# Kernel optimization log

Hardware: AMD Instinct MI355X
Metric: run time of the kernel (lower is better)

The kernel has to match this reference:

```python
import jax, jax.numpy as jnp
import numpy as np

D_MODEL, D_STATE, BATCH, SEQ = 512, 32, 8, 4096

def _hippo(n):
    i = np.arange(n)[:, None].astype(np.float64)
    j = np.arange(n)[None, :].astype(np.float64)
    P = np.where(i > j, np.sqrt(2 * i + 1) * np.sqrt(2 * j + 1), 0.0)
    P = P + np.diag(np.arange(1, n + 1).astype(np.float64))
    return (-P).astype(np.float32)

def setup_inputs() -> dict:
    key = jax.random.key(0)
    k0, k1, k2, k3 = jax.random.split(key, 4)
    x = jax.random.normal(k0, (BATCH, SEQ, D_MODEL), dtype=jnp.float32)
    A = jnp.asarray(_hippo(D_STATE))
    B = jax.random.normal(k1, (D_STATE, D_MODEL), dtype=jnp.float32) / np.float32(np.sqrt(D_MODEL))
    C = jax.random.normal(k2, (D_MODEL, D_STATE), dtype=jnp.float32) / np.float32(np.sqrt(D_STATE))
    D = jnp.ones((D_MODEL,), dtype=jnp.float32)
    log_dt = jnp.zeros((D_MODEL,), dtype=jnp.float32)
    W_out = jax.random.normal(k3, (D_MODEL, D_MODEL), dtype=jnp.float32) / np.float32(np.sqrt(D_MODEL))
    b_out = jnp.zeros((D_MODEL,), dtype=jnp.float32)
    return {"x": x, "A": A, "B": B, "C": C, "D": D, "log_dt": log_dt, "W_out": W_out, "b_out": b_out}

def reference(x, A, B, C, D, log_dt, W_out, b_out):
    # x: (b, s, d). S4 layer with bilinear discretization and tanh recurrence.
    n = A.shape[0]
    dt = jnp.mean(jnp.clip(jnp.exp(log_dt), 1e-4, 1.0))  # scalar dt.mean()
    I = jnp.eye(n, dtype=x.dtype)
    inv_term = jnp.linalg.inv(I - 0.5 * dt * A)
    A_bar = (I + 0.5 * dt * A) @ inv_term          # (n, n)
    B_bar = dt * (inv_term @ B)                    # (n, d)
    # Precompute input projection for all timesteps (vectorized):
    uB = jnp.einsum('bsd,nd->bsn', x, B_bar)       # (b, s, n)
    s0 = jnp.zeros((x.shape[0], n), dtype=x.dtype)
    def step(state, ub_t):
        state = jnp.tanh(state @ A_bar.T + ub_t)   # (b, n)
        return state, state
    final_state, states = jax.lax.scan(step, s0, jnp.swapaxes(uB, 0, 1))
    states = jnp.swapaxes(states, 0, 1)            # (b, s, n)
    y = jnp.einsum('bsn,dn->bsd', states, C) + x * D
    y = y @ W_out.T + b_out                        # output_proj (dropout = eval identity)
    return y, final_state
```

## Files before the change

### kernel.cpp

```cpp
#include <hip/hip_runtime.h>
#include <hip/hip_bf16.h>

#define D_MODEL 512
#define D_STATE 32
#define BATCH 8
#define SEQ 4096
#define MROWS (BATCH * SEQ)

typedef __bf16 bf16;
typedef __bf16 bf16x4 __attribute__((ext_vector_type(4)));
typedef __bf16 bf16x8 __attribute__((ext_vector_type(8)));
typedef float f32x4 __attribute__((ext_vector_type(4)));
typedef _Float16 half_t;
typedef _Float16 half2_t __attribute__((ext_vector_type(2)));
typedef _Float16 half8 __attribute__((ext_vector_type(8)));

#define CHUNK 16
#define BURN 80
#define NCHUNK (SEQ / CHUNK)

__device__ __forceinline__ bf16x8 cvt8(const f32x4 a, const f32x4 b) {
  bf16x8 h;
  h[0] = (bf16)a[0]; h[1] = (bf16)a[1]; h[2] = (bf16)a[2]; h[3] = (bf16)a[3];
  h[4] = (bf16)b[0]; h[5] = (bf16)b[1]; h[6] = (bf16)b[2]; h[7] = (bf16)b[3];
  return h;
}

__global__ __launch_bounds__(256) void k_pre(
    const float* __restrict__ A, const float* __restrict__ C, const float* __restrict__ Dv,
    const float* __restrict__ log_dt, const float* __restrict__ W,
    float* __restrict__ A_bar, float* __restrict__ XTs,
    bf16* __restrict__ CW, bf16* __restrict__ WD) {
  __shared__ float Xs[32][32];
  const int bid = blockIdx.x, t = threadIdx.x;
  float* Xf = &Xs[0][0];

  if (bid == 0) {
    {
      float v0 = __expf(log_dt[t]);
      float v1 = __expf(log_dt[t + 256]);
      v0 = fminf(fmaxf(v0, 1e-4f), 1.0f);
      v1 = fminf(fmaxf(v1, 1e-4f), 1.0f);
      Xf[t] = v0 + v1;
    }
    __syncthreads();
    for (int s2 = 128; s2 > 0; s2 >>= 1) {
      if (t < s2) Xf[t] += Xf[t + s2];
      __syncthreads();
    }
    const float dtv = Xf[0] * (1.0f / 512.0f);
    __syncthreads();
    {
      const int i0 = 4 * t;
      const f32x4 av = *(const f32x4*)(A + i0);
      f32x4 mv;
#pragma unroll
      for (int q = 0; q < 4; q++) {
        const int r = (i0 + q) >> 5, c = (i0 + q) & 31;
        mv[q] = (r == c ? 1.0f : 0.0f) - 0.5f * dtv * av[q];
      }
      *(f32x4*)(Xf + i0) = mv;
    }
    __syncthreads();
    if (t < 32) {
      const int j = t;
      float xcol[32];
#pragma unroll
      for (int i = 0; i < 32; i++) {
        float s0 = 0.f, s1 = 0.f, s2 = 0.f, s3 = 0.f;
#pragma unroll
        for (int k = 0; k < 32; k += 4) {
          if (k < i)     s0 -= Xf[i * 32 + k]     * xcol[k];
          if (k + 1 < i) s1 -= Xf[i * 32 + k + 1] * xcol[k + 1];
          if (k + 2 < i) s2 -= Xf[i * 32 + k + 2] * xcol[k + 2];
          if (k + 3 < i) s3 -= Xf[i * 32 + k + 3] * xcol[k + 3];
        }
        const float num = (i == j ? 1.0f : 0.0f) + ((s0 + s1) + (s2 + s3));
        xcol[i] = (i >= j) ? num / Xf[i * 32 + i] : 0.0f;
      }
#pragma unroll
      for (int i = 0; i < 32; i++) Xs[i][j] = xcol[i];
    }
    __syncthreads();
    {
      const int i0 = 4 * t;
      const int r = t >> 3;
      f32x4 ov;
#pragma unroll
      for (int q = 0; q < 4; q++) {
        const int c = (i0 + q) & 31;
        float s = 0.f;
#pragma unroll
        for (int k = 0; k < 32; k++) {
          const float p2 = (r == k ? 1.0f : 0.0f) + 0.5f * dtv * A[r * 32 + k];
          s = fmaf(p2, Xf[k * 32 + c], s);
        }
        ov[q] = s;
      }
      *(f32x4*)(A_bar + i0) = ov;
    }
#pragma unroll
    for (int i = 0; i < 4; i++) {
      const int idx = t + i * 256;
      const int k = idx >> 5, n = idx & 31;
      XTs[idx] = dtv * Xf[n * 32 + k];
    }
  } else if (bid <= 16) {
    const int w = t >> 6, lane = t & 63;
    const int l15 = lane & 15, kg = lane >> 4;
    const int m = w & 1, nf = w >> 1;
    const int eb = (bid - 1) * 32;
    const float* wp = W + (long)(eb + m * 16 + l15) * D_MODEL + kg * 8;
    const int ncol = nf * 16 + l15;
    f32x4 acc = (f32x4)(0.0f);
#pragma unroll 1
    for (int kt = 0; kt < 16; kt++) {
      const f32x4 w0 = *(const f32x4*)(wp + kt * 32);
      const f32x4 w1 = *(const f32x4*)(wp + kt * 32 + 4);
      const bf16x8 af = cvt8(w0, w1);
      bf16x8 bf;
#pragma unroll
      for (int j = 0; j < 8; j++)
        bf[j] = (bf16)C[(kt * 32 + kg * 8 + j) * D_STATE + ncol];
      acc = __builtin_amdgcn_mfma_f32_16x16x32_bf16(af, bf, acc, 0, 0, 0);
    }
#pragma unroll
    for (int jj = 0; jj < 4; jj++)
      CW[(eb + m * 16 + kg * 4 + jj) * D_STATE + ncol] = (bf16)acc[jj];
  } else {
#pragma unroll
    for (int jj = 0; jj < 16; jj++) {
      const int i = (bid - 17) * 16384 + jj * 1024 + t * 4;
      const f32x4 wv = *(const f32x4*)(W + i);
      const f32x4 dv = *(const f32x4*)(Dv + (i & 511));
      bf16x4 h;
#pragma unroll
      for (int q = 0; q < 4; q++) h[q] = (bf16)(wv[q] * dv[q]);
      *(bf16x4*)(WD + i) = h;
    }
  }
}

__device__ __forceinline__ void stage_x(const float* __restrict__ x, long rowbase,
                                        int kt, void* lds, int t) {
#pragma unroll
  for (int j = 0; j < 2; j++) {
    const int boff = j * 4096 + t * 16;
    const int r = boff >> 7;
    const int s = (boff >> 4) & 7;
    const int cb = (s ^ (r & 7)) << 4;
    const char* src = (const char*)(x + (rowbase + r) * D_MODEL) + kt * 128 + cb;
    const int udst = j * 4096 + ((t >> 6) << 10);
    __builtin_amdgcn_global_load_lds(
        (const __attribute__((address_space(1))) void*)src,
        (__attribute__((address_space(3))) void*)((char*)lds + udst), 16, 0, 0);
  }
}

__global__ __launch_bounds__(256, 2) void k_uB(
    const float* __restrict__ x, const float* __restrict__ B,
    const float* __restrict__ XTs,
    float* __restrict__ uB, bf16* __restrict__ xb) {
  __shared__ float xs[2][64 * 32];
  __shared__ float sXT[1024];
  __shared__ float srw[64 * 33];
  const int t = threadIdx.x, w = t >> 6, lane = t & 63;
  const int l15 = lane & 15, kg = lane >> 4;
  const long rowbase = (long)blockIdx.x * 64;

#pragma unroll
  for (int i = 0; i < 4; i++) sXT[t + i * 256] = XTs[t + i * 256];

  const int arow = w * 16 + l15;
  bf16* xo = xb + (rowbase + arow) * D_MODEL + kg * 8;
  const float* bp0 = B + l15 * D_MODEL + kg * 8;
  const float* bp1 = B + (16 + l15) * D_MODEL + kg * 8;
  const int ps0 = (((kg * 2) ^ (arow & 7)) << 2);
  const int ps1 = (((kg * 2 + 1) ^ (arow & 7)) << 2);
  const float* xsrow0 = &xs[0][arow * 32];
  const float* xsrow1 = &xs[1][arow * 32];

  f32x4 acc0 = (f32x4)(0.0f), acc1 = (f32x4)(0.0f);
  f32x4 cb0, cb1, cb2, cb3, nb0, nb1, nb2, nb3;

  stage_x(x, rowbase, 0, &xs[0][0], t);
  cb0 = *(const f32x4*)(bp0); cb1 = *(const f32x4*)(bp0 + 4);
  cb2 = *(const f32x4*)(bp1); cb3 = *(const f32x4*)(bp1 + 4);

#pragma unroll 1
  for (int kt = 0; kt < 16; kt++) {
    __syncthreads();
    if (kt < 15) {
      stage_x(x, rowbase, kt + 1, &xs[(kt + 1) & 1][0], t);
      const int o = (kt + 1) * 32;
      nb0 = *(const f32x4*)(bp0 + o); nb1 = *(const f32x4*)(bp0 + o + 4);
      nb2 = *(const f32x4*)(bp1 + o); nb3 = *(const f32x4*)(bp1 + o + 4);
    }
    const float* xr = (kt & 1) ? xsrow1 : xsrow0;
    const f32x4 a0 = *(const f32x4*)(xr + ps0);
    const f32x4 a1 = *(const f32x4*)(xr + ps1);
    const bf16x8 af = cvt8(a0, a1);
    *(bf16x8*)(xo + kt * 32) = af;
    const bf16x8 bh0 = cvt8(cb0, cb1);
    const bf16x8 bh1 = cvt8(cb2, cb3);
    bf16x8 bl0, bl1;
#pragma unroll
    for (int q = 0; q < 4; q++) {
      bl0[q]     = (bf16)(cb0[q] - (float)bh0[q]);
      bl0[q + 4] = (bf16)(cb1[q] - (float)bh0[q + 4]);
      bl1[q]     = (bf16)(cb2[q] - (float)bh1[q]);
      bl1[q + 4] = (bf16)(cb3[q] - (float)bh1[q + 4]);
    }
    acc0 = __builtin_amdgcn_mfma_f32_16x16x32_bf16(af, bh0, acc0, 0, 0, 0);
    acc0 = __builtin_amdgcn_mfma_f32_16x16x32_bf16(af, bl0, acc0, 0, 0, 0);
    acc1 = __builtin_amdgcn_mfma_f32_16x16x32_bf16(af, bh1, acc1, 0, 0, 0);
    acc1 = __builtin_amdgcn_mfma_f32_16x16x32_bf16(af, bl1, acc1, 0, 0, 0);
    cb0 = nb0; cb1 = nb1; cb2 = nb2; cb3 = nb3;
  }
#pragma unroll
  for (int jj = 0; jj < 4; jj++) {
    srw[(w * 16 + kg * 4 + jj) * 33 + l15]      = acc0[jj];
    srw[(w * 16 + kg * 4 + jj) * 33 + 16 + l15] = acc1[jj];
  }
  __syncthreads();
  {
    const int r = t & 63, ng = t >> 6;
    f32x4 u0 = (f32x4)(0.0f), u1 = (f32x4)(0.0f);
#pragma unroll
    for (int k = 0; k < 32; k++) {
      const float sv = srw[r * 33 + k];
      const f32x4 x0 = *(const f32x4*)&sXT[k * 32 + ng * 4];
      const f32x4 x1 = *(const f32x4*)&sXT[k * 32 + ng * 4 + 16];
#pragma unroll
      for (int q = 0; q < 4; q++) {
        u0[q] = fmaf(sv, x0[q], u0[q]);
        u1[q] = fmaf(sv, x1[q], u1[q]);
      }
    }
    float* up = uB + (rowbase + r) * D_STATE;
    *(f32x4*)(up + ng * 4) = u0;
    *(f32x4*)(up + ng * 4 + 16) = u1;
  }
}

__global__ void k_scan(const float* __restrict__ uB, const float* __restrict__ A_bar,
                       bf16* __restrict__ Sb, float* __restrict__ fs) {
  __shared__ half_t hs[256];
  const int t = threadIdx.x;
  const int g = t >> 5, n = t & 31;
  const int chain = blockIdx.x * 8 + g;
  const int b = chain >> 8;
  const int ch = chain & 255;
  const int cs = ch * CHUNK;
  const int t0 = cs - BURN;
  const int ce = cs + CHUNK;

  half2_t ah[16];
#pragma unroll
  for (int k = 0; k < 16; k++) {
    ah[k][0] = (half_t)A_bar[n * 32 + 2 * k];
    ah[k][1] = (half_t)A_bar[n * 32 + 2 * k + 1];
  }
#pragma unroll
  for (int k = 0; k < 16; k++) asm volatile("" : "+v"(ah[k]));

  const float* ub = uB + (long)b * SEQ * D_STATE + n;
  bf16* sp = Sb + ((long)b * SEQ + cs) * D_STATE + n;
  half_t* myslot = &hs[g * 32];

  float s = 0.f;
  float ubuf[8], unext[8];
#pragma unroll
  for (int i = 0; i < 8; i++) {
    const int tt = t0 + i;
    ubuf[i] = (tt >= 0) ? ub[(long)tt * D_STATE] : 0.f;
  }
  for (int tg = t0; tg < ce; tg += 8) {
    const int tn = tg + 8;
#pragma unroll
    for (int i = 0; i < 8; i++) {
      const int tt = tn + i;
      unext[i] = (tt >= 0 && tt < ce) ? ub[(long)tt * D_STATE] : 0.f;
    }
#pragma unroll
    for (int i = 0; i < 8; i++) {
      const int tt = tg + i;
      myslot[n] = (half_t)s;
      const half8 h0 = *(const half8*)(myslot + 0);
      const half8 h1 = *(const half8*)(myslot + 8);
      const half8 h2 = *(const half8*)(myslot + 16);
      const half8 h3 = *(const half8*)(myslot + 24);
      float acc0 = ubuf[i], acc1 = 0.f, acc2 = 0.f, acc3 = 0.f;
#if __has_builtin(__builtin_amdgcn_fdot2)
#pragma unroll
      for (int j = 0; j < 4; j++) {
        acc0 = __builtin_amdgcn_fdot2(ah[j],      ((const half2_t*)&h0)[j], acc0, false);
        acc1 = __builtin_amdgcn_fdot2(ah[4 + j],  ((const half2_t*)&h1)[j], acc1, false);
        acc2 = __builtin_amdgcn_fdot2(ah[8 + j],  ((const half2_t*)&h2)[j], acc2, false);
        acc3 = __builtin_amdgcn_fdot2(ah[12 + j], ((const half2_t*)&h3)[j], acc3, false);
      }
#else
#pragma unroll
      for (int j = 0; j < 4; j++) {
#pragma unroll
        for (int q = 0; q < 2; q++) {
          acc0 = fmaf((float)ah[j][q],      (float)((const half2_t*)&h0)[j][q], acc0);
          acc1 = fmaf((float)ah[4 + j][q],  (float)((const half2_t*)&h1)[j][q], acc1);
          acc2 = fmaf((float)ah[8 + j][q],  (float)((const half2_t*)&h2)[j][q], acc2);
          acc3 = fmaf((float)ah[12 + j][q], (float)((const half2_t*)&h3)[j][q], acc3);
        }
      }
#endif
      const float z = (acc0 + acc1) + (acc2 + acc3);
      const float e = __expf(2.f * z);
      const float r = __builtin_amdgcn_rcpf(e + 1.f);
      s = fmaf(-2.f, r, 1.f);
      if (tt >= cs) sp[(long)(tt - cs) * D_STATE] = (bf16)s;
    }
#pragma unroll
    for (int i = 0; i < 8; i++) ubuf[i] = unext[i];
  }
  if (ch == NCHUNK - 1) fs[b * D_STATE + n] = s;
}

__device__ __forceinline__ void stage_tile(const void* gbase, long row0, long rowStrideB,
                                           int kByte, void* lds, int w, int lane) {
#pragma unroll
  for (int j = 0; j < 2; j++) {
    const int base_off = (w << 11) + (j << 10);
    const int boff = base_off + (lane << 4);
    const int r = boff >> 6;
    const int s = (boff >> 4) & 3;
    const int cb = ((s ^ (r & 3)) << 4);
    const char* src = (const char*)gbase + (row0 + r) * rowStrideB + kByte + cb;
    __builtin_amdgcn_global_load_lds(
        (const __attribute__((address_space(1))) void*)src,
        (__attribute__((address_space(3))) void*)((char*)lds + base_off), 16, 0, 0);
  }
}

__global__ __launch_bounds__(256) void k_out(const bf16* __restrict__ xb,
                                             const bf16* __restrict__ WD,
                                             const bf16* __restrict__ Sb,
                                             const bf16* __restrict__ CW,
                                             const float* __restrict__ bias,
                                             float* __restrict__ out) {
  __shared__ bf16 As[2][128 * 32];
  __shared__ bf16 Bs[2][128 * 32];
  const int tid = threadIdx.x;
  const int w = tid >> 6, lane = tid & 63;
  const int swz = (blockIdx.x & 7) * 128 + (blockIdx.x >> 3);
  const int bm = swz >> 2, bn = swz & 3;
  const long rowbase = (long)bm * 128;
  const long colbase = (long)bn * 128;
  const int wr = w >> 1, wc = w & 1;
  const int l15 = lane & 15, kg = lane >> 4;
  const int kgs = kg ^ (l15 & 3);

  f32x4 acc[4][4];
#pragma unroll
  for (int m = 0; m < 4; m++)
#pragma unroll
    for (int n = 0; n < 4; n++) acc[m][n] = (f32x4)(0.0f);

  const int aoff = (wr * 64 + l15) * 32 + kgs * 8;
  const int boff = (wc * 64 + l15) * 32 + kgs * 8;

  auto STAGE = [&](int ti, int b) {
    if (ti < 16) {
      stage_tile(xb, rowbase, 1024, ti * 64, &As[b][0], w, lane);
      stage_tile(WD, colbase, 1024, ti * 64, &Bs[b][0], w, lane);
    } else {
      stage_tile(Sb, rowbase, 64, 0, &As[b][0], w, lane);
      stage_tile(CW, colbase, 64, 0, &Bs[b][0], w, lane);
    }
  };

  STAGE(0, 0);
  __syncthreads();
#pragma unroll 1
  for (int kt = 0; kt < 17; kt++) {
    const int cur = kt & 1;
    if (kt < 16) STAGE(kt + 1, cur ^ 1);
    bf16x8 af[4], bfr[4];
#pragma unroll
    for (int m = 0; m < 4; m++) af[m] = *(const bf16x8*)&As[cur][aoff + m * 16 * 32];
#pragma unroll
    for (int n = 0; n < 4; n++) bfr[n] = *(const bf16x8*)&Bs[cur][boff + n * 16 * 32];
#pragma unroll
    for (int m = 0; m < 4; m++)
#pragma unroll
      for (int n = 0; n < 4; n++)
        acc[m][n] = __builtin_amdgcn_mfma_f32_16x16x32_bf16(af[m], bfr[n], acc[m][n], 0, 0, 0);
    __syncthreads();
  }
#pragma unroll
  for (int n = 0; n < 4; n++) {
    const int e = (int)colbase + wc * 64 + n * 16 + l15;
    const float bv = bias[e];
#pragma unroll
    for (int m = 0; m < 4; m++) {
      const long r0 = rowbase + wr * 64 + m * 16 + kg * 4;
      const f32x4 v = acc[m][n];
#pragma unroll
      for (int jj = 0; jj < 4; jj++) out[(r0 + jj) * (long)D_MODEL + e] = v[jj] + bv;
    }
  }
}

extern "C" void kernel_launch(void* const* d_in, const int* in_sizes, int n_in,
                              void* d_out, int out_size, void* d_ws, size_t ws_size,
                              hipStream_t stream) {
  const float* x      = (const float*)d_in[0];
  const float* A      = (const float*)d_in[1];
  const float* B      = (const float*)d_in[2];
  const float* C      = (const float*)d_in[3];
  const float* Dv     = (const float*)d_in[4];
  const float* log_dt = (const float*)d_in[5];
  const float* W      = (const float*)d_in[6];
  const float* b_out  = (const float*)d_in[7];
  float* out = (float*)d_out;
  float* fs  = out + (long)MROWS * D_MODEL;

  char* ws = (char*)d_ws;
  float* A_bar = (float*)(ws + 0);
  float* XTs   = (float*)(ws + (4L << 10));
  bf16*  CW    = (bf16*)(ws + (68L << 10));
  bf16*  WD    = (bf16*)(ws + (100L << 10));
  bf16*  Sb    = (bf16*)(ws + (612L << 10));
  float* uB    = (float*)(ws + (2660L << 10));
  bf16*  xb    = (bf16*)(ws + (6756L << 10));

  k_pre<<<dim3(33), dim3(256), 0, stream>>>(A, C, Dv, log_dt, W, A_bar, XTs, CW, WD);
  k_uB<<<dim3(MROWS / 64), dim3(256), 0, stream>>>(x, B, XTs, uB, xb);
  k_scan<<<dim3(256), dim3(256), 0, stream>>>(uB, A_bar, Sb, fs);
  k_out<<<dim3((MROWS / 128) * (D_MODEL / 128)), dim3(256), 0, stream>>>(xb, WD, Sb, CW, b_out, out);
}
```

Measured before the change: 89.10 us.

## Stage wider 64-column x tiles per barrier in uB kernel and shorten burn-in

The uB projection kernel now stages 64 columns of x into LDS per phase instead of 32, halving the number of barrier-separated pipeline steps. It uses a 16-way XOR swizzle for the wider rows and raises the launch-bounds occupancy hint from 2 to 3 blocks per CU. Separately, the chunked scan's burn-in length drops from 80 to 64 steps, cutting redundant recurrence work at the risk of less accurate chunk-boundary states. Doubling the x staging buffers raises LDS use per block, which may fight the higher occupancy target.

```diff
diff --git a/kernel.cpp b/kernel.cpp
--- a/kernel.cpp
+++ b/kernel.cpp
@@ -16,7 +16,7 @@
 typedef _Float16 half8 __attribute__((ext_vector_type(8)));
 
 #define CHUNK 16
-#define BURN 80
+#define BURN 64
 #define NCHUNK (SEQ / CHUNK)
 
 __device__ __forceinline__ bf16x8 cvt8(const f32x4 a, const f32x4 b) {
@@ -141,15 +141,15 @@
   }
 }
 
-__device__ __forceinline__ void stage_x(const float* __restrict__ x, long rowbase,
-                                        int kt, void* lds, int t) {
-#pragma unroll
-  for (int j = 0; j < 2; j++) {
+__device__ __forceinline__ void stage_x2(const float* __restrict__ x, long rowbase,
+                                         int ph, void* lds, int t) {
+#pragma unroll
+  for (int j = 0; j < 4; j++) {
     const int boff = j * 4096 + t * 16;
-    const int r = boff >> 7;
-    const int s = (boff >> 4) & 7;
-    const int cb = (s ^ (r & 7)) << 4;
-    const char* src = (const char*)(x + (rowbase + r) * D_MODEL) + kt * 128 + cb;
+    const int r = boff >> 8;
+    const int s = (boff >> 4) & 15;
+    const int cb = (s ^ (r & 15)) << 4;
+    const char* src = (const char*)(x + (rowbase + r) * D_MODEL) + ph * 256 + cb;
     const int udst = j * 4096 + ((t >> 6) << 10);
     __builtin_amdgcn_global_load_lds(
         (const __attribute__((address_space(1))) void*)src,
@@ -157,11 +157,11 @@
   }
 }
 
-__global__ __launch_bounds__(256, 2) void k_uB(
+__global__ __launch_bounds__(256, 3) void k_uB(
     const float* __restrict__ x, const float* __restrict__ B,
     const float* __restrict__ XTs,
     float* __restrict__ uB, bf16* __restrict__ xb) {
-  __shared__ float xs[2][64 * 32];
+  __shared__ float xs[2][64 * 64];
   __shared__ float sXT[1024];
   __shared__ float srw[64 * 33];
   const int t = threadIdx.x, w = t >> 6, lane = t & 63;
@@ -175,47 +175,50 @@
   bf16* xo = xb + (rowbase + arow) * D_MODEL + kg * 8;
   const float* bp0 = B + l15 * D_MODEL + kg * 8;
   const float* bp1 = B + (16 + l15) * D_MODEL + kg * 8;
-  const int ps0 = (((kg * 2) ^ (arow & 7)) << 2);
-  const int ps1 = (((kg * 2 + 1) ^ (arow & 7)) << 2);
-  const float* xsrow0 = &xs[0][arow * 32];
-  const float* xsrow1 = &xs[1][arow * 32];
+  const int rkey = arow & 15;
 
   f32x4 acc0 = (f32x4)(0.0f), acc1 = (f32x4)(0.0f);
   f32x4 cb0, cb1, cb2, cb3, nb0, nb1, nb2, nb3;
 
-  stage_x(x, rowbase, 0, &xs[0][0], t);
+  stage_x2(x, rowbase, 0, &xs[0][0], t);
   cb0 = *(const f32x4*)(bp0); cb1 = *(const f32x4*)(bp0 + 4);
   cb2 = *(const f32x4*)(bp1); cb3 = *(const f32x4*)(bp1 + 4);
 
 #pragma unroll 1
-  for (int kt = 0; kt < 16; kt++) {
-    __syncthreads();
-    if (kt < 15) {
-      stage_x(x, rowbase, kt + 1, &xs[(kt + 1) & 1][0], t);
-      const int o = (kt + 1) * 32;
-      nb0 = *(const f32x4*)(bp0 + o); nb1 = *(const f32x4*)(bp0 + o + 4);
-      nb2 = *(const f32x4*)(bp1 + o); nb3 = *(const f32x4*)(bp1 + o + 4);
-    }
-    const float* xr = (kt & 1) ? xsrow1 : xsrow0;
-    const f32x4 a0 = *(const f32x4*)(xr + ps0);
-    const f32x4 a1 = *(const f32x4*)(xr + ps1);
-    const bf16x8 af = cvt8(a0, a1);
-    *(bf16x8*)(xo + kt * 32) = af;
-    const bf16x8 bh0 = cvt8(cb0, cb1);
-    const bf16x8 bh1 = cvt8(cb2, cb3);
-    bf16x8 bl0, bl1;
-#pragma unroll
-    for (int q = 0; q < 4; q++) {
-      bl0[q]     = (bf16)(cb0[q] - (float)bh0[q]);
-      bl0[q + 4] = (bf16)(cb1[q] - (float)bh0[q + 4]);
-      bl1[q]     = (bf16)(cb2[q] - (float)bh1[q]);
-      bl1[q + 4] = (bf16)(cb3[q] - (float)bh1[q + 4]);
-    }
-    acc0 = __builtin_amdgcn_mfma_f32_16x16x32_bf16(af, bh0, acc0, 0, 0, 0);
-    acc0 = __builtin_amdgcn_mfma_f32_16x16x32_bf16(af, bl0, acc0, 0, 0, 0);
-    acc1 = __builtin_amdgcn_mfma_f32_16x16x32_bf16(af, bh1, acc1, 0, 0, 0);
-    acc1 = __builtin_amdgcn_mfma_f32_16x16x32_bf16(af, bl1, acc1, 0, 0, 0);
-    cb0 = nb0; cb1 = nb1; cb2 = nb2; cb3 = nb3;
+  for (int ph = 0; ph < 8; ph++) {
+    __syncthreads();
+    if (ph < 7) stage_x2(x, rowbase, ph + 1, &xs[(ph + 1) & 1][0], t);
+    const float* xbuf = &xs[ph & 1][arow * 64];
+#pragma unroll
+    for (int h = 0; h < 2; h++) {
+      const int kt = ph * 2 + h;
+      if (kt < 15) {
+        const int o = (kt + 1) * 32;
+        nb0 = *(const f32x4*)(bp0 + o); nb1 = *(const f32x4*)(bp0 + o + 4);
+        nb2 = *(const f32x4*)(bp1 + o); nb3 = *(const f32x4*)(bp1 + o + 4);
+      }
+      const int sl0 = ((h * 8 + kg * 2) ^ rkey) << 2;
+      const int sl1 = ((h * 8 + kg * 2 + 1) ^ rkey) << 2;
+      const f32x4 a0 = *(const f32x4*)(xbuf + sl0);
+      const f32x4 a1 = *(const f32x4*)(xbuf + sl1);
+      const bf16x8 af = cvt8(a0, a1);
+      *(bf16x8*)(xo + kt * 32) = af;
+      const bf16x8 bh0 = cvt8(cb0, cb1);
+      const bf16x8 bh1 = cvt8(cb2, cb3);
+      bf16x8 bl0, bl1;
+#pragma unroll
+      for (int q = 0; q < 4; q++) {
+        bl0[q]     = (bf16)(cb0[q] - (float)bh0[q]);
+        bl0[q + 4] = (bf16)(cb1[q] - (float)bh0[q + 4]);
+        bl1[q]     = (bf16)(cb2[q] - (float)bh1[q]);
+        bl1[q + 4] = (bf16)(cb3[q] - (float)bh1[q + 4]);
+      }
+      acc0 = __builtin_amdgcn_mfma_f32_16x16x32_bf16(af, bh0, acc0, 0, 0, 0);
+      acc0 = __builtin_amdgcn_mfma_f32_16x16x32_bf16(af, bl0, acc0, 0, 0, 0);
+      acc1 = __builtin_amdgcn_mfma_f32_16x16x32_bf16(af, bh1, acc1, 0, 0, 0);
+      acc1 = __builtin_amdgcn_mfma_f32_16x16x32_bf16(af, bl1, acc1, 0, 0, 0);
+      if (kt < 15) { cb0 = nb0; cb1 = nb1; cb2 = nb2; cb3 = nb3; }
+    }
   }
 #pragma unroll
   for (int jj = 0; jj < 4; jj++) {
```

Result: no change. 89.19 us (+0.1%).
